# Kernel optimization log

Measured on AMD Instinct MI355X. Metric: run time of the kernel, lower is better.

The kernel has to match this reference:

```python
import jax, jax.numpy as jnp
import numpy as np

EPS = 1e-12  # matches torch.nn.functional.normalize default eps


def setup_inputs() -> dict:
    key = jax.random.key(0)
    k_x, k_org = jax.random.split(key)
    batch, times, d = 32, 256, 2048
    x = jax.random.normal(k_x, (batch, d, d), dtype=jnp.float32)
    # org.data.normal_(mean=0, std=0.1)
    org = 0.1 * jax.random.normal(k_org, (times, d), dtype=jnp.float32)
    return {"x": x, "org": org}


def reference(x, org):
    # F.normalize(org, dim=-1): divide each row by max(||row||_2, eps)
    norm = jnp.linalg.norm(org, axis=-1, keepdims=True)
    o = org / jnp.maximum(norm, EPS)  # (times, d)
    # Original: m = o_a (x) o_a  (rank-1 projectors, (times,d,d));
    #           y = einsum('abc,dce->dabe', m, x); trace = einsum('abcc->ab', y)
    # Algebraically: trace[batch, time] = sum_{b,c} o[a,b] * o[a,c] * x[d,c,b]
    # i.e. the quadratic form o^T x^T o per (batch, time) pair -- same math,
    # without materializing the (batch, times, d, d) intermediate.
    trace = jnp.einsum('ab,ac,dcb->da', o, o, x)  # (batch, times)
    return trace
```

## Files before the change

kernel.cpp:

```cpp
#include <hip/hip_runtime.h>
#include <hip/hip_bf16.h>

#define DDIM 2048
#define TTIMES 256
#define BM 128
#define BN 256
#define BK 32
#define NT (DDIM / BK)
#define THREADS 512
#define LDSW 40

typedef __attribute__((ext_vector_type(8))) short short8;
typedef __attribute__((ext_vector_type(4))) float f32x4;

__device__ __forceinline__ ushort f2bf(float f) {
    union { float f; unsigned int u; } v; v.f = f;
    unsigned int u = v.u;
    unsigned int r = (u + 0x7FFFu + ((u >> 16) & 1u)) >> 16;
    return (ushort)r;
}
__device__ __forceinline__ float bf2f(ushort u) {
    union { unsigned int u; float f; } v; v.u = ((unsigned int)u) << 16;
    return v.f;
}

__global__ void norm_rows(const float* __restrict__ org, ushort* __restrict__ obf) {
    const int a   = blockIdx.x;
    const int tid = threadIdx.x;
    const float* row = org + (size_t)a * DDIM;
    float4 v0 = ((const float4*)row)[tid * 2];
    float4 v1 = ((const float4*)row)[tid * 2 + 1];
    float s = v0.x*v0.x + v0.y*v0.y + v0.z*v0.z + v0.w*v0.w
            + v1.x*v1.x + v1.y*v1.y + v1.z*v1.z + v1.w*v1.w;
    #pragma unroll
    for (int off = 1; off < 64; off <<= 1) s += __shfl_xor(s, off);
    __shared__ float wsum[4];
    const int lane = tid & 63, w = tid >> 6;
    if (lane == 0) wsum[w] = s;
    __syncthreads();
    const float tot = wsum[0] + wsum[1] + wsum[2] + wsum[3];
    const float scale = 1.0f / fmaxf(sqrtf(tot), 1e-12f);
    union { ushort u[8]; uint4 v; } pk;
    pk.u[0] = f2bf(v0.x * scale); pk.u[1] = f2bf(v0.y * scale);
    pk.u[2] = f2bf(v0.z * scale); pk.u[3] = f2bf(v0.w * scale);
    pk.u[4] = f2bf(v1.x * scale); pk.u[5] = f2bf(v1.y * scale);
    pk.u[6] = f2bf(v1.z * scale); pk.u[7] = f2bf(v1.w * scale);
    ((uint4*)(obf + (size_t)a * DDIM))[tid] = pk.v;
}

__global__ __launch_bounds__(THREADS, 4) void gemm_trace(
    const float* __restrict__ x, const ushort* __restrict__ obf,
    float* __restrict__ part)
{
    __shared__ __align__(16) ushort Ab[2][BM * LDSW];
    __shared__ __align__(16) ushort Bb[2][BN * LDSW];

    const int tid  = threadIdx.x;
    const int lane = tid & 63;
    const int wid  = tid >> 6;
    const int wm   = wid >> 2;
    const int wn   = wid & 3;
    const int rb   = blockIdx.x;
    const int d    = blockIdx.y;

    const float* xtile = x + (size_t)d * DDIM * DDIM + (size_t)(rb * BM) * DDIM;

    const int ar0 = tid >> 3,         akq = tid & 7;
    const int ar1 = (tid + 512) >> 3;
    const int br0 = tid >> 2,         bkq = tid & 3;
    const int br1 = (tid + 512) >> 2;

    float4 a0 = *(const float4*)(xtile + (size_t)ar0 * DDIM + akq * 4);
    float4 a1 = *(const float4*)(xtile + (size_t)ar1 * DDIM + akq * 4);
    uint4  b0 = *(const uint4*)(obf + (size_t)br0 * DDIM + bkq * 8);
    uint4  b1 = *(const uint4*)(obf + (size_t)br1 * DDIM + bkq * 8);

    f32x4 acc[4][4];
    #pragma unroll
    for (int mi = 0; mi < 4; ++mi)
        #pragma unroll
        for (int ni = 0; ni < 4; ++ni)
            acc[mi][ni] = (f32x4){0.f, 0.f, 0.f, 0.f};

    const int lrow = lane & 15;
    const int koff = (lane >> 4) * 8;

    for (int t = 0; t < NT; ++t) {
        const int buf = t & 1;
        {
            union { ushort u[4]; uint2 v; } p;
            p.u[0] = f2bf(a0.x); p.u[1] = f2bf(a0.y); p.u[2] = f2bf(a0.z); p.u[3] = f2bf(a0.w);
            *(uint2*)&Ab[buf][ar0 * LDSW + akq * 4] = p.v;
            p.u[0] = f2bf(a1.x); p.u[1] = f2bf(a1.y); p.u[2] = f2bf(a1.z); p.u[3] = f2bf(a1.w);
            *(uint2*)&Ab[buf][ar1 * LDSW + akq * 4] = p.v;
        }
        *(uint4*)&Bb[buf][br0 * LDSW + bkq * 8] = b0;
        *(uint4*)&Bb[buf][br1 * LDSW + bkq * 8] = b1;
        __syncthreads();
        if (t + 1 < NT) {
            const float*  xk = xtile + (t + 1) * BK;
            const ushort* ok = obf   + (t + 1) * BK;
            a0 = *(const float4*)(xk + (size_t)ar0 * DDIM + akq * 4);
            a1 = *(const float4*)(xk + (size_t)ar1 * DDIM + akq * 4);
            b0 = *(const uint4*)(ok + (size_t)br0 * DDIM + bkq * 8);
            b1 = *(const uint4*)(ok + (size_t)br1 * DDIM + bkq * 8);
        }
        short8 af[4], bfr[4];
        #pragma unroll
        for (int mi = 0; mi < 4; ++mi)
            af[mi] = *(const short8*)&Ab[buf][(wm * 64 + mi * 16 + lrow) * LDSW + koff];
        #pragma unroll
        for (int ni = 0; ni < 4; ++ni)
            bfr[ni] = *(const short8*)&Bb[buf][(wn * 64 + ni * 16 + lrow) * LDSW + koff];
        #pragma unroll
        for (int mi = 0; mi < 4; ++mi)
            #pragma unroll
            for (int ni = 0; ni < 4; ++ni)
                acc[mi][ni] = __builtin_amdgcn_mfma_f32_16x16x32_bf16(
                    af[mi], bfr[ni], acc[mi][ni], 0, 0, 0);
    }

    __syncthreads();
    float* plds = (float*)&Ab[0][0];

    #pragma unroll
    for (int ni = 0; ni < 4; ++ni) {
        const int a_idx = wn * 64 + ni * 16 + lrow;
        float ps = 0.f;
        #pragma unroll
        for (int mi = 0; mi < 4; ++mi) {
            const int bg = rb * BM + wm * 64 + mi * 16 + (lane >> 4) * 4;
            const ushort4 w = *(const ushort4*)(obf + (size_t)a_idx * DDIM + bg);
            ps += bf2f(w.x) * acc[mi][ni][0];
            ps += bf2f(w.y) * acc[mi][ni][1];
            ps += bf2f(w.z) * acc[mi][ni][2];
            ps += bf2f(w.w) * acc[mi][ni][3];
        }
        ps += __shfl_xor(ps, 16);
        ps += __shfl_xor(ps, 32);
        if (lane < 16) plds[wm * 256 + a_idx] = ps;
    }
    __syncthreads();
    if (tid < 256) {
        const float v = plds[tid] + plds[256 + tid];
        part[((size_t)(d * 16) + rb) * 256 + tid] = v;
    }
}

__global__ void reduce_part(const float* __restrict__ part, float* __restrict__ out) {
    const int d = blockIdx.x;
    const int a = threadIdx.x;
    float s = 0.f;
    #pragma unroll
    for (int rb = 0; rb < 16; ++rb)
        s += part[((size_t)(d * 16) + rb) * 256 + a];
    out[(size_t)d * 256 + a] = s;
}

extern "C" void kernel_launch(void* const* d_in, const int* in_sizes, int n_in,
                              void* d_out, int out_size, void* d_ws, size_t ws_size,
                              hipStream_t stream) {
    const float* x   = (const float*)d_in[0];
    const float* org = (const float*)d_in[1];
    float* out = (float*)d_out;

    ushort* obf = (ushort*)d_ws;
    float*  prt = (float*)((char*)d_ws + (1 << 20));

    norm_rows<<<dim3(TTIMES), dim3(256), 0, stream>>>(org, obf);
    gemm_trace<<<dim3(DDIM / BM, 32), dim3(THREADS), 0, stream>>>(x, obf, prt);
    reduce_part<<<dim3(32), dim3(256), 0, stream>>>(prt, out);
}
```

Before: 158.4 us.

## Drop LDS staging; load MFMA fragments directly from global with register double-buffering

Removes the shared-memory tiles and barriers from the GEMM. Each wave now loads its A (fp32 x) and B (bf16 o) fragments straight from global into registers in MFMA layout, converting to bf16 on the fly, and ping-pongs two register sets so loads overlap compute. Block shape shrinks to 256 threads covering a 64-row slab with 4 waves, doubling the number of partial sums the reduce kernel must add. The trade-off is no inter-wave reuse of x through LDS: all 4 waves in a block read the same x rows, so more global/L2 traffic and strided row accesses, plus higher register pressure.

```diff
diff --git a/kernel.cpp b/kernel.cpp
--- a/kernel.cpp
+++ b/kernel.cpp
@@ -3,12 +3,7 @@
 
 #define DDIM 2048
 #define TTIMES 256
-#define BM 128
-#define BN 256
-#define BK 32
-#define NT (DDIM / BK)
-#define THREADS 512
-#define LDSW 40
+#define NT 64
 
 typedef __attribute__((ext_vector_type(8))) short short8;
 typedef __attribute__((ext_vector_type(4))) float f32x4;
@@ -22,6 +17,11 @@
 __device__ __forceinline__ float bf2f(ushort u) {
     union { unsigned int u; float f; } v; v.u = ((unsigned int)u) << 16;
     return v.f;
+}
+__device__ __forceinline__ short cvt1(float f) {
+    union { __hip_bfloat16 h; ushort u; } cv;
+    cv.h = __float2bfloat16(f);
+    return (short)cv.u;
 }
 
 __global__ void norm_rows(const float* __restrict__ org, ushort* __restrict__ obf) {
@@ -48,32 +48,22 @@
     ((uint4*)(obf + (size_t)a * DDIM))[tid] = pk.v;
 }
 
-__global__ __launch_bounds__(THREADS, 4) void gemm_trace(
+__global__ __launch_bounds__(256, 3) void gemm_trace(
     const float* __restrict__ x, const ushort* __restrict__ obf,
     float* __restrict__ part)
 {
-    __shared__ __align__(16) ushort Ab[2][BM * LDSW];
-    __shared__ __align__(16) ushort Bb[2][BN * LDSW];
-
     const int tid  = threadIdx.x;
     const int lane = tid & 63;
-    const int wid  = tid >> 6;
-    const int wm   = wid >> 2;
-    const int wn   = wid & 3;
+    const int wn   = tid >> 6;
     const int rb   = blockIdx.x;
     const int d    = blockIdx.y;
 
-    const float* xtile = x + (size_t)d * DDIM * DDIM + (size_t)(rb * BM) * DDIM;
+    const int lr = lane & 15;
+    const int lq = lane >> 4;
 
-    const int ar0 = tid >> 3,         akq = tid & 7;
-    const int ar1 = (tid + 512) >> 3;
-    const int br0 = tid >> 2,         bkq = tid & 3;
-    const int br1 = (tid + 512) >> 2;
-
-    float4 a0 = *(const float4*)(xtile + (size_t)ar0 * DDIM + akq * 4);
-    float4 a1 = *(const float4*)(xtile + (size_t)ar1 * DDIM + akq * 4);
-    uint4  b0 = *(const uint4*)(obf + (size_t)br0 * DDIM + bkq * 8);
-    uint4  b1 = *(const uint4*)(obf + (size_t)br1 * DDIM + bkq * 8);
+    const float*  ap = x + (size_t)d * DDIM * DDIM
+                         + (size_t)(rb * 64 + lr) * DDIM + lq * 8;
+    const ushort* bp = obf + (size_t)(wn * 64 + lr) * DDIM + lq * 8;
 
     f32x4 acc[4][4];
     #pragma unroll
@@ -82,54 +72,53 @@
         for (int ni = 0; ni < 4; ++ni)
             acc[mi][ni] = (f32x4){0.f, 0.f, 0.f, 0.f};
 
-    const int lrow = lane & 15;
-    const int koff = (lane >> 4) * 8;
+#define LOADT(AS, BS, t) do {                                               \
+    _Pragma("unroll")                                                       \
+    for (int mi = 0; mi < 4; ++mi) {                                        \
+        const float* p_ = ap + (size_t)mi * 16 * DDIM + (t) * 32;           \
+        AS[mi][0] = *(const float4*)p_;                                     \
+        AS[mi][1] = *(const float4*)(p_ + 4);                               \
+    }                                                                       \
+    _Pragma("unroll")                                                       \
+    for (int ni = 0; ni < 4; ++ni)                                          \
+        BS[ni] = *(const uint4*)(bp + (size_t)ni * 16 * DDIM + (t) * 32);   \
+} while (0)
 
-    for (int t = 0; t < NT; ++t) {
-        const int buf = t & 1;
-        {
-            union { ushort u[4]; uint2 v; } p;
-            p.u[0] = f2bf(a0.x); p.u[1] = f2bf(a0.y); p.u[2] = f2bf(a0.z); p.u[3] = f2bf(a0.w);
-            *(uint2*)&Ab[buf][ar0 * LDSW + akq * 4] = p.v;
-            p.u[0] = f2bf(a1.x); p.u[1] = f2bf(a1.y); p.u[2] = f2bf(a1.z); p.u[3] = f2bf(a1.w);
-            *(uint2*)&Ab[buf][ar1 * LDSW + akq * 4] = p.v;
-        }
-        *(uint4*)&Bb[buf][br0 * LDSW + bkq * 8] = b0;
-        *(uint4*)&Bb[buf][br1 * LDSW + bkq * 8] = b1;
-        __syncthreads();
-        if (t + 1 < NT) {
-            const float*  xk = xtile + (t + 1) * BK;
-            const ushort* ok = obf   + (t + 1) * BK;
-            a0 = *(const float4*)(xk + (size_t)ar0 * DDIM + akq * 4);
-            a1 = *(const float4*)(xk + (size_t)ar1 * DDIM + akq * 4);
-            b0 = *(const uint4*)(ok + (size_t)br0 * DDIM + bkq * 8);
-            b1 = *(const uint4*)(ok + (size_t)br1 * DDIM + bkq * 8);
-        }
-        short8 af[4], bfr[4];
-        #pragma unroll
-        for (int mi = 0; mi < 4; ++mi)
-            af[mi] = *(const short8*)&Ab[buf][(wm * 64 + mi * 16 + lrow) * LDSW + koff];
-        #pragma unroll
-        for (int ni = 0; ni < 4; ++ni)
-            bfr[ni] = *(const short8*)&Bb[buf][(wn * 64 + ni * 16 + lrow) * LDSW + koff];
-        #pragma unroll
-        for (int mi = 0; mi < 4; ++mi)
-            #pragma unroll
-            for (int ni = 0; ni < 4; ++ni)
-                acc[mi][ni] = __builtin_amdgcn_mfma_f32_16x16x32_bf16(
-                    af[mi], bfr[ni], acc[mi][ni], 0, 0, 0);
+#define CMPT(AS, BS) do {                                                   \
+    _Pragma("unroll")                                                       \
+    for (int mi = 0; mi < 4; ++mi) {                                        \
+        short8 af_;                                                         \
+        af_[0] = cvt1(AS[mi][0].x); af_[1] = cvt1(AS[mi][0].y);             \
+        af_[2] = cvt1(AS[mi][0].z); af_[3] = cvt1(AS[mi][0].w);             \
+        af_[4] = cvt1(AS[mi][1].x); af_[5] = cvt1(AS[mi][1].y);             \
+        af_[6] = cvt1(AS[mi][1].z); af_[7] = cvt1(AS[mi][1].w);             \
+        _Pragma("unroll")                                                   \
+        for (int ni = 0; ni < 4; ++ni)                                      \
+            acc[mi][ni] = __builtin_amdgcn_mfma_f32_16x16x32_bf16(          \
+                af_, *(const short8*)&BS[ni], acc[mi][ni], 0, 0, 0);        \
+    }                                                                       \
+} while (0)
+
+    float4 aA[4][2], aB[4][2];
+    uint4  bA[4],   bB[4];
+
+    LOADT(aA, bA, 0);
+    for (int t = 0; t < NT; t += 2) {
+        LOADT(aB, bB, t + 1);
+        CMPT(aA, bA);
+        if (t + 2 < NT) LOADT(aA, bA, t + 2);
+        CMPT(aB, bB);
     }
-
-    __syncthreads();
-    float* plds = (float*)&Ab[0][0];
+#undef LOADT
+#undef CMPT
 
     #pragma unroll
     for (int ni = 0; ni < 4; ++ni) {
-        const int a_idx = wn * 64 + ni * 16 + lrow;
+        const int a_idx = wn * 64 + ni * 16 + lr;
         float ps = 0.f;
         #pragma unroll
         for (int mi = 0; mi < 4; ++mi) {
-            const int bg = rb * BM + wm * 64 + mi * 16 + (lane >> 4) * 4;
+            const int bg = rb * 64 + mi * 16 + lq * 4;
             const ushort4 w = *(const ushort4*)(obf + (size_t)a_idx * DDIM + bg);
             ps += bf2f(w.x) * acc[mi][ni][0];
             ps += bf2f(w.y) * acc[mi][ni][1];
@@ -138,12 +127,8 @@
         }
         ps += __shfl_xor(ps, 16);
         ps += __shfl_xor(ps, 32);
-        if (lane < 16) plds[wm * 256 + a_idx] = ps;
-    }
-    __syncthreads();
-    if (tid < 256) {
-        const float v = plds[tid] + plds[256 + tid];
-        part[((size_t)(d * 16) + rb) * 256 + tid] = v;
+        if (lane < 16)
+            part[((size_t)d * 32 + rb) * TTIMES + a_idx] = ps;
     }
 }
 
@@ -152,9 +137,9 @@
     const int a = threadIdx.x;
     float s = 0.f;
     #pragma unroll
-    for (int rb = 0; rb < 16; ++rb)
-        s += part[((size_t)(d * 16) + rb) * 256 + a];
-    out[(size_t)d * 256 + a] = s;
+    for (int rb = 0; rb < 32; ++rb)
+        s += part[((size_t)d * 32 + rb) * TTIMES + a];
+    out[(size_t)d * TTIMES + a] = s;
 }
 
 extern "C" void kernel_launch(void* const* d_in, const int* in_sizes, int n_in,
@@ -168,6 +153,6 @@
     float*  prt = (float*)((char*)d_ws + (1 << 20));
 
     norm_rows<<<dim3(TTIMES), dim3(256), 0, stream>>>(org, obf);
-    gemm_trace<<<dim3(DDIM / BM, 32), dim3(THREADS), 0, stream>>>(x, obf, prt);
+    gemm_trace<<<dim3(32, 32), dim3(256), 0, stream>>>(x, obf, prt);
     reduce_part<<<dim3(32), dim3(256), 0, stream>>>(prt, out);
 }
```

Result: slower. 394.4 us (+149.0%).

## Stage GEMM tiles via direct global-to-LDS loads with XOR swizzle

Applied to the files above, without the earlier changes.

Replaces register-staged global loads with global_load_lds DMA into LDS, keeping x as fp32 in LDS and converting to bf16 after the LDS read. An XOR swizzle replaces the padded LDS layout to avoid bank conflicts, and manual vmcnt waits plus raw barriers pipeline the next tile's load behind the current MFMAs. The aim is to cut register pressure and VGPR round-trips on the load path. In exchange, fp32 x doubles LDS traffic and footprint for A, and conversion now happens per wave, redundantly across the wn waves.

```diff
diff --git a/kernel.cpp b/kernel.cpp
--- a/kernel.cpp
+++ b/kernel.cpp
@@ -3,15 +3,18 @@
 
 #define DDIM 2048
 #define TTIMES 256
-#define BM 128
-#define BN 256
-#define BK 32
-#define NT (DDIM / BK)
+#define NT 64
 #define THREADS 512
-#define LDSW 40
 
 typedef __attribute__((ext_vector_type(8))) short short8;
 typedef __attribute__((ext_vector_type(4))) float f32x4;
+
+using gvoid = const __attribute__((address_space(1))) void;
+using svoid = __attribute__((address_space(3))) void;
+
+__device__ __forceinline__ void gld16(const void* g, void* l) {
+    __builtin_amdgcn_global_load_lds((gvoid*)g, (svoid*)l, 16, 0, 0);
+}
 
 __device__ __forceinline__ ushort f2bf(float f) {
     union { float f; unsigned int u; } v; v.f = f;
@@ -22,6 +25,11 @@
 __device__ __forceinline__ float bf2f(ushort u) {
     union { unsigned int u; float f; } v; v.u = ((unsigned int)u) << 16;
     return v.f;
+}
+__device__ __forceinline__ short cvt1(float f) {
+    union { __hip_bfloat16 h; ushort u; } cv;
+    cv.h = __float2bfloat16(f);
+    return (short)cv.u;
 }
 
 __global__ void norm_rows(const float* __restrict__ org, ushort* __restrict__ obf) {
@@ -52,8 +60,8 @@
     const float* __restrict__ x, const ushort* __restrict__ obf,
     float* __restrict__ part)
 {
-    __shared__ __align__(16) ushort Ab[2][BM * LDSW];
-    __shared__ __align__(16) ushort Bb[2][BN * LDSW];
+    __shared__ __align__(16) char Ab[2][16384];
+    __shared__ __align__(16) char Bb[2][16384];
 
     const int tid  = threadIdx.x;
     const int lane = tid & 63;
@@ -63,17 +71,41 @@
     const int rb   = blockIdx.x;
     const int d    = blockIdx.y;
 
-    const float* xtile = x + (size_t)d * DDIM * DDIM + (size_t)(rb * BM) * DDIM;
-
-    const int ar0 = tid >> 3,         akq = tid & 7;
-    const int ar1 = (tid + 512) >> 3;
-    const int br0 = tid >> 2,         bkq = tid & 3;
-    const int br1 = (tid + 512) >> 2;
-
-    float4 a0 = *(const float4*)(xtile + (size_t)ar0 * DDIM + akq * 4);
-    float4 a1 = *(const float4*)(xtile + (size_t)ar1 * DDIM + akq * 4);
-    uint4  b0 = *(const uint4*)(obf + (size_t)br0 * DDIM + bkq * 8);
-    uint4  b1 = *(const uint4*)(obf + (size_t)br1 * DDIM + bkq * 8);
+    const char* ab = (const char*)(x + (size_t)d * DDIM * DDIM + (size_t)rb * 128 * DDIM);
+    const char* bb = (const char*)obf;
+
+    const int ar0 = tid >> 3,         aq0 = ((tid & 7) ^ (ar0 & 7)) * 16;
+    const int ar1 = (tid + 512) >> 3, aq1 = (((tid + 512) & 7) ^ (ar1 & 7)) * 16;
+    const int br0 = tid >> 2,         bq0 = ((tid & 3) ^ (br0 & 3)) * 16;
+    const int br1 = (tid + 512) >> 2, bq1 = (((tid + 512) & 3) ^ (br1 & 3)) * 16;
+
+    const char* as0 = ab + (size_t)ar0 * (DDIM * 4) + aq0;
+    const char* as1 = ab + (size_t)ar1 * (DDIM * 4) + aq1;
+    const char* bs0 = bb + (size_t)br0 * (DDIM * 2) + bq0;
+    const char* bs1 = bb + (size_t)br1 * (DDIM * 2) + bq1;
+
+#define STAGE(t, buf) do {                                \
+    gld16(as0 + (t) * 128, &Ab[buf][tid * 16]);           \
+    gld16(as1 + (t) * 128, &Ab[buf][(tid + 512) * 16]);   \
+    gld16(bs0 + (t) * 64,  &Bb[buf][tid * 16]);           \
+    gld16(bs1 + (t) * 64,  &Bb[buf][(tid + 512) * 16]);   \
+} while (0)
+
+    const int lr = lane & 15;
+    const int lq = lane >> 4;
+
+    int aoff0[4], aoff1[4], boff[4];
+    #pragma unroll
+    for (int mi = 0; mi < 4; ++mi) {
+        const int r = wm * 64 + mi * 16 + lr;
+        aoff0[mi] = r * 128 + ((2 * lq)     ^ (r & 7)) * 16;
+        aoff1[mi] = r * 128 + ((2 * lq + 1) ^ (r & 7)) * 16;
+    }
+    #pragma unroll
+    for (int ni = 0; ni < 4; ++ni) {
+        const int rt = wn * 64 + ni * 16 + lr;
+        boff[ni] = rt * 64 + (lq ^ (rt & 3)) * 16;
+    }
 
     f32x4 acc[4][4];
     #pragma unroll
@@ -82,54 +114,54 @@
         for (int ni = 0; ni < 4; ++ni)
             acc[mi][ni] = (f32x4){0.f, 0.f, 0.f, 0.f};
 
-    const int lrow = lane & 15;
-    const int koff = (lane >> 4) * 8;
-
+    STAGE(0, 0);
     for (int t = 0; t < NT; ++t) {
-        const int buf = t & 1;
-        {
-            union { ushort u[4]; uint2 v; } p;
-            p.u[0] = f2bf(a0.x); p.u[1] = f2bf(a0.y); p.u[2] = f2bf(a0.z); p.u[3] = f2bf(a0.w);
-            *(uint2*)&Ab[buf][ar0 * LDSW + akq * 4] = p.v;
-            p.u[0] = f2bf(a1.x); p.u[1] = f2bf(a1.y); p.u[2] = f2bf(a1.z); p.u[3] = f2bf(a1.w);
-            *(uint2*)&Ab[buf][ar1 * LDSW + akq * 4] = p.v;
+        const int cur = t & 1;
+        if (t + 1 < NT) {
+            STAGE(t + 1, cur ^ 1);
+            asm volatile("s_waitcnt vmcnt(4)" ::: "memory");
+        } else {
+            asm volatile("s_waitcnt vmcnt(0)" ::: "memory");
         }
-        *(uint4*)&Bb[buf][br0 * LDSW + bkq * 8] = b0;
-        *(uint4*)&Bb[buf][br1 * LDSW + bkq * 8] = b1;
-        __syncthreads();
-        if (t + 1 < NT) {
-            const float*  xk = xtile + (t + 1) * BK;
-            const ushort* ok = obf   + (t + 1) * BK;
-            a0 = *(const float4*)(xk + (size_t)ar0 * DDIM + akq * 4);
-            a1 = *(const float4*)(xk + (size_t)ar1 * DDIM + akq * 4);
-            b0 = *(const uint4*)(ok + (size_t)br0 * DDIM + bkq * 8);
-            b1 = *(const uint4*)(ok + (size_t)br1 * DDIM + bkq * 8);
+        __builtin_amdgcn_sched_barrier(0);
+        __builtin_amdgcn_s_barrier();
+        __builtin_amdgcn_sched_barrier(0);
+
+        short8 af[4], bfr[4];
+        #pragma unroll
+        for (int mi = 0; mi < 4; ++mi) {
+            const float4 lo = *(const float4*)&Ab[cur][aoff0[mi]];
+            const float4 hi = *(const float4*)&Ab[cur][aoff1[mi]];
+            short8 a8;
+            a8[0] = cvt1(lo.x); a8[1] = cvt1(lo.y); a8[2] = cvt1(lo.z); a8[3] = cvt1(lo.w);
+            a8[4] = cvt1(hi.x); a8[5] = cvt1(hi.y); a8[6] = cvt1(hi.z); a8[7] = cvt1(hi.w);
+            af[mi] = a8;
         }
-        short8 af[4], bfr[4];
-        #pragma unroll
-        for (int mi = 0; mi < 4; ++mi)
-            af[mi] = *(const short8*)&Ab[buf][(wm * 64 + mi * 16 + lrow) * LDSW + koff];
         #pragma unroll
         for (int ni = 0; ni < 4; ++ni)
-            bfr[ni] = *(const short8*)&Bb[buf][(wn * 64 + ni * 16 + lrow) * LDSW + koff];
+            bfr[ni] = *(const short8*)&Bb[cur][boff[ni]];
         #pragma unroll
         for (int mi = 0; mi < 4; ++mi)
             #pragma unroll
             for (int ni = 0; ni < 4; ++ni)
                 acc[mi][ni] = __builtin_amdgcn_mfma_f32_16x16x32_bf16(
                     af[mi], bfr[ni], acc[mi][ni], 0, 0, 0);
-    }
-
-    __syncthreads();
+
+        __builtin_amdgcn_sched_barrier(0);
+        __builtin_amdgcn_s_barrier();
+        __builtin_amdgcn_sched_barrier(0);
+    }
+#undef STAGE
+
     float* plds = (float*)&Ab[0][0];
 
     #pragma unroll
     for (int ni = 0; ni < 4; ++ni) {
-        const int a_idx = wn * 64 + ni * 16 + lrow;
+        const int a_idx = wn * 64 + ni * 16 + lr;
         float ps = 0.f;
         #pragma unroll
         for (int mi = 0; mi < 4; ++mi) {
-            const int bg = rb * BM + wm * 64 + mi * 16 + (lane >> 4) * 4;
+            const int bg = rb * 128 + wm * 64 + mi * 16 + lq * 4;
             const ushort4 w = *(const ushort4*)(obf + (size_t)a_idx * DDIM + bg);
             ps += bf2f(w.x) * acc[mi][ni][0];
             ps += bf2f(w.y) * acc[mi][ni][1];
@@ -141,10 +173,8 @@
         if (lane < 16) plds[wm * 256 + a_idx] = ps;
     }
     __syncthreads();
-    if (tid < 256) {
-        const float v = plds[tid] + plds[256 + tid];
-        part[((size_t)(d * 16) + rb) * 256 + tid] = v;
-    }
+    if (tid < 256)
+        part[((size_t)d * 16 + rb) * TTIMES + tid] = plds[tid] + plds[256 + tid];
 }
 
 __global__ void reduce_part(const float* __restrict__ part, float* __restrict__ out) {
@@ -153,8 +183,8 @@
     float s = 0.f;
     #pragma unroll
     for (int rb = 0; rb < 16; ++rb)
-        s += part[((size_t)(d * 16) + rb) * 256 + a];
-    out[(size_t)d * 256 + a] = s;
+        s += part[((size_t)d * 16 + rb) * TTIMES + a];
+    out[(size_t)d * TTIMES + a] = s;
 }
 
 extern "C" void kernel_launch(void* const* d_in, const int* in_sizes, int n_in,
@@ -168,6 +198,6 @@
     float*  prt = (float*)((char*)d_ws + (1 << 20));
 
     norm_rows<<<dim3(TTIMES), dim3(256), 0, stream>>>(org, obf);
-    gemm_trace<<<dim3(DDIM / BM, 32), dim3(THREADS), 0, stream>>>(x, obf, prt);
+    gemm_trace<<<dim3(16, 32), dim3(THREADS), 0, stream>>>(x, obf, prt);
     reduce_part<<<dim3(32), dim3(256), 0, stream>>>(prt, out);
 }
```

After: 151.5 us. -4.3%, faster.
